# Kernel optimization log

Measured on AMD Instinct MI355X. Metric: run time of the kernel, lower is better.

## Reference

```python
import jax, jax.numpy as jnp
import numpy as np

N, E, DIN, HID, DOUT = 50000, 800000, 128, 128, 64
NEG_SLOPE = 0.2


def setup_inputs() -> dict:
    key = jax.random.key(0)
    ks = jax.random.split(key, 16)
    x = jax.random.normal(ks[0], (N, DIN), dtype=jnp.float32)
    edge_index = jax.random.randint(ks[1], (2, E), 0, N, dtype=jnp.int64)

    def lin(k, fan_in, fan_out):
        kw, kb = jax.random.split(k)
        s = 1.0 / np.sqrt(fan_in)
        W = jax.random.uniform(kw, (fan_in, fan_out), jnp.float32, -s, s)
        b = jax.random.uniform(kb, (fan_out,), jnp.float32, -s, s)
        return W, b

    Wl, bl = lin(ks[2], DIN, DIN)   # GATv2 lin_l
    Wr, br = lin(ks[3], DIN, DIN)   # GATv2 lin_r
    att = jax.random.uniform(ks[4], (DIN,), jnp.float32, -1.0 / np.sqrt(DIN), 1.0 / np.sqrt(DIN))
    bg = jnp.zeros((DIN,), jnp.float32)  # GAT output bias
    W1, b1 = lin(ks[5], DIN, HID)   # ChebConv K=1 -> plain linear
    W2, b2 = lin(ks[6], HID, HID)
    W3, b3 = lin(ks[7], HID, DOUT)
    return {"x": x, "edge_index": edge_index, "Wl": Wl, "bl": bl, "Wr": Wr,
            "br": br, "att": att, "bg": bg, "W1": W1, "b1": b1,
            "W2": W2, "b2": b2, "W3": W3, "b3": b3}


def reference(x, edge_index, Wl, bl, Wr, br, att, bg, W1, b1, W2, b2, W3, b3):
    n = x.shape[0]
    # GATv2Conv adds self loops by default
    loop = jnp.arange(n, dtype=edge_index.dtype)
    src = jnp.concatenate([edge_index[0], loop])  # source j
    dst = jnp.concatenate([edge_index[1], loop])  # target i

    xl = x @ Wl + bl  # [N, DIN]
    xr = x @ Wr + br  # [N, DIN]

    # GATv2 edge scores: leaky_relu(x_l[j] + x_r[i]) . att
    e = jax.nn.leaky_relu(xl[src] + xr[dst], NEG_SLOPE)  # [E+N, DIN]
    a = e @ att                                          # [E+N]

    # softmax over incoming edges of each destination node
    amax = jax.ops.segment_max(a, dst, num_segments=n)
    ea = jnp.exp(a - amax[dst])
    denom = jax.ops.segment_sum(ea, dst, num_segments=n)
    alpha = ea / denom[dst]                              # [E+N]

    # aggregate messages alpha * x_l[j] at destinations
    h = jax.ops.segment_sum(alpha[:, None] * xl[src], dst, num_segments=n) + bg

    # ChebConv with K=1 reduces to a linear layer (T_0(L) = I)
    h = jax.nn.relu(h @ W1 + b1)
    h = jax.nn.relu(h @ W2 + b2)
    # dropout_rate = 0.0 -> identity
    return h @ W3 + b3
```

## Files before the change

kernel.cpp:

```cpp
#include <hip/hip_runtime.h>
#include <hip/hip_bf16.h>

#define DIN 128
#define NEG_SLOPE 0.2f
#define PTILE 2048
#define FCAP 8192
#define CVT_BLKS 289

typedef __attribute__((ext_vector_type(8))) short bf16x8;
typedef __attribute__((ext_vector_type(8))) unsigned short u16x8;
typedef __attribute__((ext_vector_type(4))) float f32x4;
typedef __attribute__((ext_vector_type(2))) float f32x2;
typedef __attribute__((ext_vector_type(4))) unsigned int u32x4;

__device__ __forceinline__ ushort f2bf(float f) {
  unsigned u = __float_as_uint(f);
  u += 0x7FFFu + ((u >> 16) & 1u);
  return (ushort)(u >> 16);
}
__device__ __forceinline__ float bf2f(ushort u) {
  return __uint_as_float((unsigned)u << 16);
}
__device__ __forceinline__ f32x2 bfpair(unsigned u) {
  f32x2 r;
  r.x = __uint_as_float(u << 16);
  r.y = __uint_as_float(u & 0xFFFF0000u);
  return r;
}

template <int CTRL>
__device__ __forceinline__ float dppadd(float x) {
  int v = __builtin_amdgcn_update_dpp(0, __float_as_int(x), CTRL, 0xf, 0xf, true);
  return x + __int_as_float(v);
}
__device__ __forceinline__ float red16(float t) {
  t = dppadd<0xB1>(t);
  t = dppadd<0x4E>(t);
  t = dppadd<0x141>(t);
  t = dppadd<0x140>(t);
  return t;
}

__global__ __launch_bounds__(256) void cvt_hist_kernel(
    const float* __restrict__ Wl, const float* __restrict__ Wr,
    const float* __restrict__ W1, const float* __restrict__ W2,
    const float* __restrict__ W3,
    ushort* __restrict__ WlT, ushort* __restrict__ WrT,
    ushort* __restrict__ W1T, ushort* __restrict__ W2T,
    ushort* __restrict__ W3T,
    const int* __restrict__ ei, int* __restrict__ ghist, int E) {
  if (blockIdx.x < CVT_BLKS) {
    int i = blockIdx.x * 256 + threadIdx.x;
    if (i < 16384) {
      int k = i >> 7, c = i & 127; WlT[c * 128 + k] = f2bf(Wl[i]);
    } else if (i < 32768) {
      int j = i - 16384; int k = j >> 7, c = j & 127; WrT[c * 128 + k] = f2bf(Wr[j]);
    } else if (i < 49152) {
      int j = i - 32768; int k = j >> 7, c = j & 127; W1T[c * 128 + k] = f2bf(W1[j]);
    } else if (i < 65536) {
      int j = i - 49152; int k = j >> 7, c = j & 127; W2T[c * 128 + k] = f2bf(W2[j]);
    } else if (i < 73728) {
      int j = i - 65536; int k = j >> 6, c = j & 63; W3T[c * 128 + k] = f2bf(W3[j]);
    }
  } else {
    __shared__ int h[256];
    h[threadIdx.x] = 0;
    __syncthreads();
    int tile = blockIdx.x - CVT_BLKS;
    for (int e = tile * PTILE + threadIdx.x;
         e < min(E, (tile + 1) * PTILE); e += 256)
      atomicAdd(&h[ei[E + e] >> 8], 1);
    __syncthreads();
    if (h[threadIdx.x] > 0) atomicAdd(&ghist[threadIdx.x], h[threadIdx.x]);
  }
}

__global__ __launch_bounds__(256) void scan_small_kernel(
    const int* __restrict__ ghist, int* __restrict__ cum,
    int* __restrict__ cursor) {
  __shared__ int sh[256];
  int tid = threadIdx.x;
  int v = ghist[tid];
  sh[tid] = v;
  __syncthreads();
  for (int d = 1; d < 256; d <<= 1) {
    int t = (tid >= d) ? sh[tid - d] : 0;
    __syncthreads();
    sh[tid] += t;
    __syncthreads();
  }
  int exc = sh[tid] - v;
  cum[tid] = exc;
  cursor[tid] = exc;
  if (tid == 255) cum[256] = sh[255];
}

__global__ __launch_bounds__(256) void lin_partition_kernel(
    const float* __restrict__ x,
    const ushort* __restrict__ WlT, const float* __restrict__ bl,
    const ushort* __restrict__ WrT, const float* __restrict__ br,
    ushort* __restrict__ xl, ushort* __restrict__ xr, int n, int nblk_lin,
    const int* __restrict__ ei, unsigned* __restrict__ part,
    int* __restrict__ cursor, int E) {
  if ((int)blockIdx.x < nblk_lin) {
    const int tid = threadIdx.x;
    const int wv = tid >> 6, lane = tid & 63;
    const int m = lane & 15, quad = lane >> 4;
    const int colbase = (wv & 1) * 64;
    const int nodew = blockIdx.x * 32 + (wv >> 1) * 16;
    int arow = nodew + m; if (arow >= n) arow = n - 1;
    f32x4 accl[4], accr[4];
#pragma unroll
    for (int nt = 0; nt < 4; nt++) { accl[nt] = (f32x4){0,0,0,0}; accr[nt] = (f32x4){0,0,0,0}; }
#pragma unroll
    for (int kk = 0; kk < 4; kk++) {
      int k0 = kk * 32 + quad * 8;
      const float4* xp = (const float4*)(x + (long)arow * 128 + k0);
      float4 x0 = xp[0], x1 = xp[1];
      bf16x8 af;
      af[0] = (short)f2bf(x0.x); af[1] = (short)f2bf(x0.y);
      af[2] = (short)f2bf(x0.z); af[3] = (short)f2bf(x0.w);
      af[4] = (short)f2bf(x1.x); af[5] = (short)f2bf(x1.y);
      af[6] = (short)f2bf(x1.z); af[7] = (short)f2bf(x1.w);
#pragma unroll
      for (int nt = 0; nt < 4; nt++) {
        int brow = colbase + nt * 16 + m;
        bf16x8 bl8 = *(const bf16x8*)(WlT + brow * 128 + k0);
        bf16x8 br8 = *(const bf16x8*)(WrT + brow * 128 + k0);
        accl[nt] = __builtin_amdgcn_mfma_f32_16x16x32_bf16(af, bl8, accl[nt], 0, 0, 0);
        accr[nt] = __builtin_amdgcn_mfma_f32_16x16x32_bf16(af, br8, accr[nt], 0, 0, 0);
      }
    }
#pragma unroll
    for (int nt = 0; nt < 4; nt++) {
      int col = colbase + nt * 16 + m;
      float vbl = bl[col], vbr = br[col];
#pragma unroll
      for (int r = 0; r < 4; r++) {
        int node = nodew + quad * 4 + r;
        if (node < n) {
          xl[(long)node * 128 + col] = f2bf(accl[nt][r] + vbl);
          xr[(long)node * 128 + col] = f2bf(accr[nt][r] + vbr);
        }
      }
    }
  } else {
    __shared__ int hist[256], pref[256], sexcl[256], curs[256], gbase[256];
    __shared__ unsigned buf[PTILE];
    const int tid = threadIdx.x;
    const int tile0 = ((int)blockIdx.x - nblk_lin) * PTILE;
    const int tcount = min(PTILE, E - tile0);
    hist[tid] = 0;
    __syncthreads();
    unsigned pk[PTILE / 256];
    int cnt = 0;
    for (int i = tid; i < tcount; i += 256) {
      int e = tile0 + i;
      int s = ei[e], d = ei[E + e];
      unsigned p = ((unsigned)d << 16) | (unsigned)s;
      pk[cnt++] = p;
      atomicAdd(&hist[d >> 8], 1);
    }
    __syncthreads();
    int v = hist[tid];
    pref[tid] = v;
    __syncthreads();
    for (int d = 1; d < 256; d <<= 1) {
      int t = (tid >= d) ? pref[tid - d] : 0;
      __syncthreads();
      pref[tid] += t;
      __syncthreads();
    }
    int exc = pref[tid] - v;
    sexcl[tid] = exc;
    curs[tid] = exc;
    gbase[tid] = (v > 0) ? atomicAdd(&cursor[tid], v) : 0;
    __syncthreads();
    for (int j = 0; j < cnt; j++) {
      int b = pk[j] >> 24;
      int pos = atomicAdd(&curs[b], 1);
      buf[pos] = pk[j];
    }
    __syncthreads();
    for (int i = tid; i < tcount; i += 256) {
      unsigned p = buf[i];
      int b = p >> 24;
      part[gbase[b] + (i - sexcl[b])] = p;
    }
  }
}

__global__ __launch_bounds__(512) void fine_kernel(
    const unsigned* __restrict__ part, const int* __restrict__ cum,
    int* __restrict__ offsets, ushort* __restrict__ ssrc,
    int N, int E, int nbuck) {
  __shared__ int hist[256], pref[256], curs[256];
  __shared__ unsigned buf[FCAP], buf2[FCAP];
  const int tid = threadIdx.x;
  const int b = blockIdx.x;
  const int seg0 = cum[b];
  const int len = min(cum[b + 1] - seg0, FCAP);
  if (tid < 256) hist[tid] = 0;
  __syncthreads();
  for (int i = tid; i < len; i += 512) {
    unsigned p = part[seg0 + i];
    buf[i] = p;
    atomicAdd(&hist[(p >> 16) & 255], 1);
  }
  __syncthreads();
  int v = (tid < 256) ? hist[tid] : 0;
  if (tid < 256) pref[tid] = v;
  __syncthreads();
  for (int d = 1; d < 256; d <<= 1) {
    int t = (tid >= d && tid < 256) ? pref[tid - d] : 0;
    __syncthreads();
    if (tid < 256) pref[tid] += t;
    __syncthreads();
  }
  if (tid < 256) {
    int exc = pref[tid] - v;
    curs[tid] = exc;
    int node = b * 256 + tid;
    if (node < N) offsets[node] = seg0 + exc;
  }
  if (b == nbuck - 1 && tid == 0) offsets[N] = E;
  __syncthreads();
  for (int i = tid; i < len; i += 512) {
    unsigned p = buf[i];
    int pos = atomicAdd(&curs[(p >> 16) & 255], 1);
    buf2[pos] = p;
  }
  __syncthreads();
  for (int i = tid; i < len; i += 512)
    ssrc[seg0 + i] = (ushort)(buf2[i] & 0xFFFFu);
}

__global__ __launch_bounds__(256) void node_aggr_kernel(
    const ushort* __restrict__ xl, const ushort* __restrict__ xr,
    const float* __restrict__ att, const float* __restrict__ bg,
    const int* __restrict__ offsets, const ushort* __restrict__ ssrc,
    ushort* __restrict__ h, int n) {
  int wave = (int)((blockIdx.x * (long)blockDim.x + threadIdx.x) >> 6);
  int lane = threadIdx.x & 63;
  if (wave >= n) return;
  const int node = wave;
  const int eg = lane >> 4, sl = lane & 15;
  f32x2 av2[4], r2[4], acc2[4];
  {
    const float4* ap = (const float4*)(att + sl * 8);
    float4 a0 = ap[0], a1 = ap[1];
    av2[0] = (f32x2){a0.x, a0.y}; av2[1] = (f32x2){a0.z, a0.w};
    av2[2] = (f32x2){a1.x, a1.y}; av2[3] = (f32x2){a1.z, a1.w};
  }
  const ushort* __restrict__ xls = xl + sl * 8;
  u32x4 rv = *(const u32x4*)(xr + (long)node * 128 + sl * 8);
  u32x4 lv = *(const u32x4*)(xls + (long)node * 128);
  float denom;
  {
    f32x2 t2 = {0.f, 0.f};
    f32x2 l2[4];
#pragma unroll
    for (int jp = 0; jp < 4; jp++) {
      r2[jp] = bfpair(rv[jp]);
      l2[jp] = bfpair(lv[jp]);
      f32x2 v = l2[jp] + r2[jp];
      t2 += __builtin_elementwise_max(v, NEG_SLOPE * v) * av2[jp];
    }
    float t = red16(t2.x + t2.y);
    float es = __expf(t);
    denom = (eg == 0) ? es : 0.f;
#pragma unroll
    for (int jp = 0; jp < 4; jp++)
      acc2[jp] = (eg == 0) ? es * l2[jp] : (f32x2){0.f, 0.f};
  }
  const int beg = offsets[node];
  const int end = offsets[node + 1];
  int ia = beg + 2 * eg;
  bool va = ia < end, vb = ia + 1 < end;
  int sa = va ? (int)ssrc[ia] : node;
  int sb = vb ? (int)ssrc[ia + 1] : node;
  u32x4 uva = *(const u32x4*)(xls + (long)sa * 128);
  u32x4 uvb = *(const u32x4*)(xls + (long)sb * 128);
  for (int p = beg; p < end; p += 8) {
    u32x4 ca = uva, cb = uvb;
    bool cva = va, cvb = vb;
    int ian = p + 8 + 2 * eg;
    va = ian < end; vb = ian + 1 < end;
    sa = va ? (int)ssrc[ian] : node;
    sb = vb ? (int)ssrc[ian + 1] : node;
    uva = *(const u32x4*)(xls + (long)sa * 128);
    uvb = *(const u32x4*)(xls + (long)sb * 128);
    f32x2 ua2[4], ub2[4];
    f32x2 ta2 = {0.f, 0.f}, tb2 = {0.f, 0.f};
#pragma unroll
    for (int jp = 0; jp < 4; jp++) {
      ua2[jp] = bfpair(ca[jp]);
      ub2[jp] = bfpair(cb[jp]);
      f32x2 va2 = ua2[jp] + r2[jp];
      f32x2 vb2 = ub2[jp] + r2[jp];
      ta2 += __builtin_elementwise_max(va2, NEG_SLOPE * va2) * av2[jp];
      tb2 += __builtin_elementwise_max(vb2, NEG_SLOPE * vb2) * av2[jp];
    }
    float ta = red16(ta2.x + ta2.y);
    float tb = red16(tb2.x + tb2.y);
    float ea = cva ? __expf(ta) : 0.f;
    float eb = cvb ? __expf(tb) : 0.f;
    denom += ea + eb;
#pragma unroll
    for (int jp = 0; jp < 4; jp++)
      acc2[jp] += ea * ua2[jp] + eb * ub2[jp];
  }
#pragma unroll
  for (int jp = 0; jp < 4; jp++) {
    acc2[jp].x += __shfl_xor(acc2[jp].x, 16);
    acc2[jp].y += __shfl_xor(acc2[jp].y, 16);
    acc2[jp].x += __shfl_xor(acc2[jp].x, 32);
    acc2[jp].y += __shfl_xor(acc2[jp].y, 32);
  }
  denom += __shfl_xor(denom, 16);
  denom += __shfl_xor(denom, 32);
  if (eg == 0) {
    float inv = 1.0f / denom;
    const float4* bp = (const float4*)(bg + sl * 8);
    float4 g0 = bp[0], g1 = bp[1];
    f32x2 gv[4] = {{g0.x, g0.y}, {g0.z, g0.w}, {g1.x, g1.y}, {g1.z, g1.w}};
    u16x8 o;
#pragma unroll
    for (int jp = 0; jp < 4; jp++) {
      f32x2 hv = acc2[jp] * inv + gv[jp];
      o[2 * jp]     = f2bf(hv.x);
      o[2 * jp + 1] = f2bf(hv.y);
    }
    *(u16x8*)(h + (long)node * 128 + sl * 8) = o;
  }
}

#define LDSP 136
__global__ __launch_bounds__(256) void mlp_mfma_kernel(
    const ushort* __restrict__ hb,
    const ushort* __restrict__ W1T, const float* __restrict__ b1,
    const ushort* __restrict__ W2T, const float* __restrict__ b2,
    const ushort* __restrict__ W3T, const float* __restrict__ b3,
    float* __restrict__ out, int n) {
  __shared__ ushort act[32][LDSP];
  const int tid = threadIdx.x;
  const int wv = tid >> 6, lane = tid & 63;
  const int m = lane & 15, quad = lane >> 4;
  const int half = wv & 1, ng = wv >> 1;
  const int colbase = half * 64;
  const int nodew = blockIdx.x * 32 + ng * 16;
  int arow = nodew + m; if (arow >= n) arow = n - 1;
  f32x4 acc[4];
#pragma unroll
  for (int nt = 0; nt < 4; nt++) acc[nt] = (f32x4){0,0,0,0};
#pragma unroll
  for (int kk = 0; kk < 4; kk++) {
    int k0 = kk * 32 + quad * 8;
    bf16x8 af = *(const bf16x8*)(hb + (long)arow * 128 + k0);
#pragma unroll
    for (int nt = 0; nt < 4; nt++) {
      bf16x8 b8 = *(const bf16x8*)(W1T + (colbase + nt * 16 + m) * 128 + k0);
      acc[nt] = __builtin_amdgcn_mfma_f32_16x16x32_bf16(af, b8, acc[nt], 0, 0, 0);
    }
  }
#pragma unroll
  for (int nt = 0; nt < 4; nt++) {
    int col = colbase + nt * 16 + m;
    float b = b1[col];
#pragma unroll
    for (int r = 0; r < 4; r++)
      act[ng * 16 + quad * 4 + r][col] = f2bf(fmaxf(acc[nt][r] + b, 0.f));
  }
  __syncthreads();
#pragma unroll
  for (int nt = 0; nt < 4; nt++) acc[nt] = (f32x4){0,0,0,0};
#pragma unroll
  for (int kk = 0; kk < 4; kk++) {
    int k0 = kk * 32 + quad * 8;
    bf16x8 af = *(const bf16x8*)(&act[ng * 16 + m][k0]);
#pragma unroll
    for (int nt = 0; nt < 4; nt++) {
      bf16x8 b8 = *(const bf16x8*)(W2T + (colbase + nt * 16 + m) * 128 + k0);
      acc[nt] = __builtin_amdgcn_mfma_f32_16x16x32_bf16(af, b8, acc[nt], 0, 0, 0);
    }
  }
  __syncthreads();
#pragma unroll
  for (int nt = 0; nt < 4; nt++) {
    int col = colbase + nt * 16 + m;
    float b = b2[col];
#pragma unroll
    for (int r = 0; r < 4; r++)
      act[ng * 16 + quad * 4 + r][col] = f2bf(fmaxf(acc[nt][r] + b, 0.f));
  }
  __syncthreads();
  f32x4 acc3[2];
#pragma unroll
  for (int nt = 0; nt < 2; nt++) acc3[nt] = (f32x4){0,0,0,0};
#pragma unroll
  for (int kk = 0; kk < 4; kk++) {
    int k0 = kk * 32 + quad * 8;
    bf16x8 af = *(const bf16x8*)(&act[ng * 16 + m][k0]);
#pragma unroll
    for (int nt = 0; nt < 2; nt++) {
      bf16x8 b8 = *(const bf16x8*)(W3T + (half * 32 + nt * 16 + m) * 128 + k0);
      acc3[nt] = __builtin_amdgcn_mfma_f32_16x16x32_bf16(af, b8, acc3[nt], 0, 0, 0);
    }
  }
#pragma unroll
  for (int nt = 0; nt < 2; nt++) {
    int col = half * 32 + nt * 16 + m;
    float b = b3[col];
#pragma unroll
    for (int r = 0; r < 4; r++) {
      int node = nodew + quad * 4 + r;
      if (node < n) out[(long)node * 64 + col] = acc3[nt][r] + b;
    }
  }
}

extern "C" void kernel_launch(void* const* d_in, const int* in_sizes, int n_in,
                              void* d_out, int out_size, void* d_ws, size_t ws_size,
                              hipStream_t stream) {
  const float* x   = (const float*)d_in[0];
  const int*   ei  = (const int*)d_in[1];
  const float* Wl  = (const float*)d_in[2];
  const float* bl  = (const float*)d_in[3];
  const float* Wr  = (const float*)d_in[4];
  const float* br  = (const float*)d_in[5];
  const float* att = (const float*)d_in[6];
  const float* bg  = (const float*)d_in[7];
  const float* W1  = (const float*)d_in[8];
  const float* b1  = (const float*)d_in[9];
  const float* W2  = (const float*)d_in[10];
  const float* b2  = (const float*)d_in[11];
  const float* W3  = (const float*)d_in[12];
  const float* b3  = (const float*)d_in[13];
  float* out = (float*)d_out;

  const int N = in_sizes[0] / DIN;
  const int E = in_sizes[1] / 2;
  const int nbuck = (N + 255) >> 8;

  char* ws = (char*)d_ws;
  size_t off = 0;
  auto alloc = [&](size_t bytes) {
    void* p = ws + off;
    off += (bytes + 255) & ~(size_t)255;
    return p;
  };
  int* ghist     = (int*)alloc(256 * 4);
  int* cum       = (int*)alloc(257 * 4);
  int* cursor    = (int*)alloc(256 * 4);
  int* offsets   = (int*)alloc(((size_t)N + 4) * 4);
  unsigned* part = (unsigned*)alloc((size_t)E * 4);
  ushort* ssrc   = (ushort*)alloc(((size_t)E + 16) * 2);
  ushort* xlb    = (ushort*)alloc((size_t)N * DIN * 2);
  ushort* xrb    = (ushort*)alloc((size_t)N * DIN * 2);
  ushort* hbf    = (ushort*)alloc((size_t)N * DIN * 2);
  ushort* WlT    = (ushort*)alloc(16384 * 2);
  ushort* WrT    = (ushort*)alloc(16384 * 2);
  ushort* W1T    = (ushort*)alloc(16384 * 2);
  ushort* W2T    = (ushort*)alloc(16384 * 2);
  ushort* W3T    = (ushort*)alloc(8192 * 2);
  (void)ws_size;

  hipMemsetAsync(ghist, 0, 256 * 4, stream);

  int ntile = (E + PTILE - 1) / PTILE;
  cvt_hist_kernel<<<CVT_BLKS + ntile, 256, 0, stream>>>(
      Wl, Wr, W1, W2, W3, WlT, WrT, W1T, W2T, W3T, ei, ghist, E);

  scan_small_kernel<<<1, 256, 0, stream>>>(ghist, cum, cursor);

  int nblk32 = (N + 31) / 32;
  lin_partition_kernel<<<nblk32 + ntile, 256, 0, stream>>>(
      x, WlT, bl, WrT, br, xlb, xrb, N, nblk32, ei, part, cursor, E);

  fine_kernel<<<nbuck, 512, 0, stream>>>(part, cum, offsets, ssrc, N, E, nbuck);

  int nwblk = (N + 3) / 4;
  node_aggr_kernel<<<nwblk, 256, 0, stream>>>(xlb, xrb, att, bg,
                                              offsets, ssrc, hbf, N);

  mlp_mfma_kernel<<<nblk32, 256, 0, stream>>>(hbf, W1T, b1, W2T, b2,
                                              W3T, b3, out, N);
}
```

Baseline: 238.2 us.

## Pre-convert x to bf16, use packed f32 math, hoist neighbor prefetch

```diff
diff --git a/kernel.cpp b/kernel.cpp
--- a/kernel.cpp
+++ b/kernel.cpp
@@ -18,14 +18,27 @@
   u += 0x7FFFu + ((u >> 16) & 1u);
   return (ushort)(u >> 16);
 }
-__device__ __forceinline__ float bf2f(ushort u) {
-  return __uint_as_float((unsigned)u << 16);
-}
 __device__ __forceinline__ f32x2 bfpair(unsigned u) {
   f32x2 r;
   r.x = __uint_as_float(u << 16);
   r.y = __uint_as_float(u & 0xFFFF0000u);
   return r;
+}
+
+__device__ __forceinline__ f32x2 pk_add(f32x2 a, f32x2 b) {
+  f32x2 d;
+  asm("v_pk_add_f32 %0, %1, %2" : "=v"(d) : "v"(a), "v"(b));
+  return d;
+}
+__device__ __forceinline__ f32x2 pk_mul(f32x2 a, f32x2 b) {
+  f32x2 d;
+  asm("v_pk_mul_f32 %0, %1, %2" : "=v"(d) : "v"(a), "v"(b));
+  return d;
+}
+__device__ __forceinline__ f32x2 pk_fma(f32x2 a, f32x2 b, f32x2 c) {
+  f32x2 d;
+  asm("v_pk_fma_f32 %0, %1, %2, %3" : "=v"(d) : "v"(a), "v"(b), "v"(c));
+  return d;
 }
 
 template <int CTRL>
@@ -42,6 +55,7 @@
 }
 
 __global__ __launch_bounds__(256) void cvt_hist_kernel(
+    const float* __restrict__ x, ushort* __restrict__ xbf, int xblk, long ntot,
     const float* __restrict__ Wl, const float* __restrict__ Wr,
     const float* __restrict__ W1, const float* __restrict__ W2,
     const float* __restrict__ W3,
@@ -49,8 +63,20 @@
     ushort* __restrict__ W1T, ushort* __restrict__ W2T,
     ushort* __restrict__ W3T,
     const int* __restrict__ ei, int* __restrict__ ghist, int E) {
-  if (blockIdx.x < CVT_BLKS) {
-    int i = blockIdx.x * 256 + threadIdx.x;
+  if ((int)blockIdx.x < xblk) {
+    long i = (long)blockIdx.x * 2048 + threadIdx.x * 8;
+    if (i + 8 <= ntot) {
+      const float4* xp = (const float4*)(x + i);
+      float4 f0 = xp[0], f1 = xp[1];
+      u16x8 o;
+      o[0] = f2bf(f0.x); o[1] = f2bf(f0.y); o[2] = f2bf(f0.z); o[3] = f2bf(f0.w);
+      o[4] = f2bf(f1.x); o[5] = f2bf(f1.y); o[6] = f2bf(f1.z); o[7] = f2bf(f1.w);
+      *(u16x8*)(xbf + i) = o;
+    } else {
+      for (long j = i; j < ntot; j++) xbf[j] = f2bf(x[j]);
+    }
+  } else if ((int)blockIdx.x < xblk + CVT_BLKS) {
+    int i = ((int)blockIdx.x - xblk) * 256 + threadIdx.x;
     if (i < 16384) {
       int k = i >> 7, c = i & 127; WlT[c * 128 + k] = f2bf(Wl[i]);
     } else if (i < 32768) {
@@ -66,7 +92,7 @@
     __shared__ int h[256];
     h[threadIdx.x] = 0;
     __syncthreads();
-    int tile = blockIdx.x - CVT_BLKS;
+    int tile = (int)blockIdx.x - xblk - CVT_BLKS;
     for (int e = tile * PTILE + threadIdx.x;
          e < min(E, (tile + 1) * PTILE); e += 256)
       atomicAdd(&h[ei[E + e] >> 8], 1);
@@ -96,7 +122,7 @@
 }
 
 __global__ __launch_bounds__(256) void lin_partition_kernel(
-    const float* __restrict__ x,
+    const ushort* __restrict__ xbf,
     const ushort* __restrict__ WlT, const float* __restrict__ bl,
     const ushort* __restrict__ WrT, const float* __restrict__ br,
     ushort* __restrict__ xl, ushort* __restrict__ xr, int n, int nblk_lin,
@@ -115,13 +141,7 @@
 #pragma unroll
     for (int kk = 0; kk < 4; kk++) {
       int k0 = kk * 32 + quad * 8;
-      const float4* xp = (const float4*)(x + (long)arow * 128 + k0);
-      float4 x0 = xp[0], x1 = xp[1];
-      bf16x8 af;
-      af[0] = (short)f2bf(x0.x); af[1] = (short)f2bf(x0.y);
-      af[2] = (short)f2bf(x0.z); af[3] = (short)f2bf(x0.w);
-      af[4] = (short)f2bf(x1.x); af[5] = (short)f2bf(x1.y);
-      af[6] = (short)f2bf(x1.z); af[7] = (short)f2bf(x1.w);
+      bf16x8 af = *(const bf16x8*)(xbf + (long)arow * 128 + k0);
 #pragma unroll
       for (int nt = 0; nt < 4; nt++) {
         int brow = colbase + nt * 16 + m;
@@ -245,6 +265,18 @@
   if (wave >= n) return;
   const int node = wave;
   const int eg = lane >> 4, sl = lane & 15;
+  const int beg = offsets[node];
+  const int end = offsets[node + 1];
+  const int last = end - 1;
+  const ushort* __restrict__ xls = xl + sl * 8;
+  int ia = beg + 2 * eg;
+  bool va = ia < end, vb = ia + 1 < end;
+  int sa = (int)ssrc[min(ia, last)];
+  int sb = (int)ssrc[min(ia + 1, last)];
+  u32x4 uva = *(const u32x4*)(xls + (long)sa * 128);
+  u32x4 uvb = *(const u32x4*)(xls + (long)sb * 128);
+
+  const f32x2 ns2 = {NEG_SLOPE, NEG_SLOPE};
   f32x2 av2[4], r2[4], acc2[4];
   {
     const float4* ap = (const float4*)(att + sl * 8);
@@ -252,7 +284,6 @@
     av2[0] = (f32x2){a0.x, a0.y}; av2[1] = (f32x2){a0.z, a0.w};
     av2[2] = (f32x2){a1.x, a1.y}; av2[3] = (f32x2){a1.z, a1.w};
   }
-  const ushort* __restrict__ xls = xl + sl * 8;
   u32x4 rv = *(const u32x4*)(xr + (long)node * 128 + sl * 8);
   u32x4 lv = *(const u32x4*)(xls + (long)node * 128);
   float denom;
@@ -263,8 +294,10 @@
     for (int jp = 0; jp < 4; jp++) {
       r2[jp] = bfpair(rv[jp]);
       l2[jp] = bfpair(lv[jp]);
-      f32x2 v = l2[jp] + r2[jp];
-      t2 += __builtin_elementwise_max(v, NEG_SLOPE * v) * av2[jp];
+      f32x2 v = pk_add(l2[jp], r2[jp]);
+      f32x2 w = pk_mul(ns2, v);
+      f32x2 mm = __builtin_elementwise_max(v, w);
+      t2 = pk_fma(mm, av2[jp], t2);
     }
     float t = red16(t2.x + t2.y);
     float es = __expf(t);
@@ -273,21 +306,13 @@
     for (int jp = 0; jp < 4; jp++)
       acc2[jp] = (eg == 0) ? es * l2[jp] : (f32x2){0.f, 0.f};
   }
-  const int beg = offsets[node];
-  const int end = offsets[node + 1];
-  int ia = beg + 2 * eg;
-  bool va = ia < end, vb = ia + 1 < end;
-  int sa = va ? (int)ssrc[ia] : node;
-  int sb = vb ? (int)ssrc[ia + 1] : node;
-  u32x4 uva = *(const u32x4*)(xls + (long)sa * 128);
-  u32x4 uvb = *(const u32x4*)(xls + (long)sb * 128);
   for (int p = beg; p < end; p += 8) {
     u32x4 ca = uva, cb = uvb;
     bool cva = va, cvb = vb;
     int ian = p + 8 + 2 * eg;
     va = ian < end; vb = ian + 1 < end;
-    sa = va ? (int)ssrc[ian] : node;
-    sb = vb ? (int)ssrc[ian + 1] : node;
+    sa = (int)ssrc[min(ian, last)];
+    sb = (int)ssrc[min(ian + 1, last)];
     uva = *(const u32x4*)(xls + (long)sa * 128);
     uvb = *(const u32x4*)(xls + (long)sb * 128);
     f32x2 ua2[4], ub2[4];
@@ -296,19 +321,24 @@
     for (int jp = 0; jp < 4; jp++) {
       ua2[jp] = bfpair(ca[jp]);
       ub2[jp] = bfpair(cb[jp]);
-      f32x2 va2 = ua2[jp] + r2[jp];
-      f32x2 vb2 = ub2[jp] + r2[jp];
-      ta2 += __builtin_elementwise_max(va2, NEG_SLOPE * va2) * av2[jp];
-      tb2 += __builtin_elementwise_max(vb2, NEG_SLOPE * vb2) * av2[jp];
+      f32x2 va2 = pk_add(ua2[jp], r2[jp]);
+      f32x2 vb2 = pk_add(ub2[jp], r2[jp]);
+      f32x2 wa2 = pk_mul(ns2, va2);
+      f32x2 wb2 = pk_mul(ns2, vb2);
+      f32x2 ma2 = __builtin_elementwise_max(va2, wa2);
+      f32x2 mb2 = __builtin_elementwise_max(vb2, wb2);
+      ta2 = pk_fma(ma2, av2[jp], ta2);
+      tb2 = pk_fma(mb2, av2[jp], tb2);
     }
     float ta = red16(ta2.x + ta2.y);
     float tb = red16(tb2.x + tb2.y);
     float ea = cva ? __expf(ta) : 0.f;
     float eb = cvb ? __expf(tb) : 0.f;
     denom += ea + eb;
+    f32x2 eap = {ea, ea}, ebp = {eb, eb};
 #pragma unroll
     for (int jp = 0; jp < 4; jp++)
-      acc2[jp] += ea * ua2[jp] + eb * ub2[jp];
+      acc2[jp] = pk_fma(eap, ua2[jp], pk_fma(ebp, ub2[jp], acc2[jp]));
   }
 #pragma unroll
   for (int jp = 0; jp < 4; jp++) {
@@ -464,18 +494,22 @@
   ushort* W2T    = (ushort*)alloc(16384 * 2);
   ushort* W3T    = (ushort*)alloc(8192 * 2);
   (void)ws_size;
+  ushort* xbf = hbf;
 
   hipMemsetAsync(ghist, 0, 256 * 4, stream);
 
+  long ntot = (long)N * DIN;
+  int xblk = (int)((ntot + 2047) / 2048);
   int ntile = (E + PTILE - 1) / PTILE;
-  cvt_hist_kernel<<<CVT_BLKS + ntile, 256, 0, stream>>>(
+  cvt_hist_kernel<<<xblk + CVT_BLKS + ntile, 256, 0, stream>>>(
+      x, xbf, xblk, ntot,
       Wl, Wr, W1, W2, W3, WlT, WrT, W1T, W2T, W3T, ei, ghist, E);
 
   scan_small_kernel<<<1, 256, 0, stream>>>(ghist, cum, cursor);
 
   int nblk32 = (N + 31) / 32;
   lin_partition_kernel<<<nblk32 + ntile, 256, 0, stream>>>(
-      x, WlT, bl, WrT, br, xlb, xrb, N, nblk32, ei, part, cursor, E);
+      xbf, WlT, bl, WrT, br, xlb, xrb, N, nblk32, ei, part, cursor, E);
 
   fine_kernel<<<nbuck, 512, 0, stream>>>(part, cum, offsets, ssrc, N, E, nbuck);
 
```

Result: slower. 249.3 us (+4.7%).
